# Kernel tuning notes

Measured on AMD Instinct MI355X. Metric: run time of the kernel, lower is better.

## Reference

```python
import jax, jax.numpy as jnp
import numpy as np

B, T, C, HS = 8, 4096, 1024, 64
HALF = HS // 2
ROPE_BASE = 10000.0


def _rope_tables(t_len, half_dim, base=ROPE_BASE):
    inv_freq = base ** (-jnp.arange(half_dim, dtype=jnp.float32) / half_dim)
    freqs = jnp.arange(t_len, dtype=jnp.float32)[:, None] * inv_freq[None, :]  # (T, D/2)
    return jnp.cos(freqs), jnp.sin(freqs)


def apply_rope(x, cos, sin):
    # x: (B, T, D) with interleaved even/odd pairs; cos/sin: (T, D/2)
    x_even = x[..., ::2]
    x_odd = x[..., 1::2]
    r_even = x_even * cos[None] - x_odd * sin[None]
    r_odd = x_even * sin[None] + x_odd * cos[None]
    # re-interleave
    return jnp.stack([r_even, r_odd], axis=-1).reshape(x.shape)


def setup_inputs() -> dict:
    key = jax.random.key(0)
    kx, kq, kk, kv = jax.random.split(key, 4)
    s = 1.0 / np.sqrt(C)
    cos, sin = _rope_tables(T, HALF)
    return {
        "x": jax.random.normal(kx, (B, T, C), dtype=jnp.float32),
        "cos": cos,
        "sin": sin,
        "Wq": jax.random.normal(kq, (C, HS), dtype=jnp.float32) * s,
        "Wk": jax.random.normal(kk, (C, HS), dtype=jnp.float32) * s,
        "Wv": jax.random.normal(kv, (C, HS), dtype=jnp.float32) * s,
    }


def reference(x, cos, sin, Wq, Wk, Wv):
    # q/k/v projections (bias-free Linear)
    q = jnp.einsum('btc,cd->btd', x, Wq)
    k = jnp.einsum('btc,cd->btd', x, Wk)
    v = jnp.einsum('btc,cd->btd', x, Wv)
    q = apply_rope(q, cos, sin)
    k = apply_rope(k, cos, sin)
    t = x.shape[1]
    scale = 1.0 / jnp.sqrt(jnp.asarray(k.shape[-1], dtype=x.dtype))
    wei = jnp.einsum('bqd,bkd->bqk', q, k) * scale  # (B, T, T)
    causal = jnp.tril(jnp.ones((t, t), dtype=bool))
    wei = jnp.where(causal[None], wei, -jnp.inf)
    wei = jax.nn.softmax(wei, axis=-1)
    # dropout = 0.0 (eval mode)
    return jnp.einsum('bqk,bkd->bqd', wei, v)
```

## Files before the change

kernel.cpp:

```cpp
#include <hip/hip_runtime.h>
#include <hip/hip_bf16.h>

#define BB 8
#define TT 4096
#define CC 1024
#define HS 64

typedef __attribute__((ext_vector_type(8))) __bf16 bf16x8;
typedef __attribute__((ext_vector_type(4))) __bf16 bf16x4;
typedef __attribute__((ext_vector_type(4))) float f32x4;

static __device__ __forceinline__ unsigned pack_bf16(float a, float b) {
    unsigned short ua = __builtin_bit_cast(unsigned short, (__bf16)a);
    unsigned short ub = __builtin_bit_cast(unsigned short, (__bf16)b);
    return (unsigned)ua | ((unsigned)ub << 16);
}

__global__ __launch_bounds__(256) void wprep_kernel(
    const float* __restrict__ Wq, const float* __restrict__ Wk,
    const float* __restrict__ Wv, __bf16* __restrict__ Wt)
{
    int i = blockIdx.x * 256 + threadIdx.x;
    int dr = i >> 10;
    int c  = i & 1023;
    int m  = dr >> 6;
    int d  = dr & 63;
    const float* src = (m == 0) ? Wq : ((m == 1) ? Wk : Wv);
    float v = src[(long)c * HS + d];
    if (m == 0) v *= 0.125f * 1.4426950408889634f;
    Wt[i] = (__bf16)v;
}

__global__ __launch_bounds__(256) void qkv_rope_kernel(
    const float* __restrict__ x,
    const float* __restrict__ cosT,
    const float* __restrict__ sinT,
    const __bf16* __restrict__ Wt,
    __bf16* __restrict__ Qo, __bf16* __restrict__ Ko, __bf16* __restrict__ Vo)
{
    __shared__ __bf16 xs[64][72];
    __shared__ __bf16 Wl[192][72];

    const int tid  = threadIdx.x;
    const int lane = tid & 63;
    const int w    = tid >> 6;
    const int col  = lane & 15;
    const int grp  = lane >> 4;
    const long rowbase = (long)blockIdx.x * 64;

    f32x4 acc[12];
#pragma unroll
    for (int i = 0; i < 12; i++) acc[i] = 0.0f;

    for (int ck = 0; ck < CC; ck += 64) {
        {
            int r = tid >> 2, c0 = (tid & 3) * 16;
            const float4* src = (const float4*)(x + (rowbase + r) * (long)CC + ck + c0);
#pragma unroll
            for (int i = 0; i < 4; i++) {
                float4 v = src[i];
                bf16x4 t;
                t[0] = (__bf16)v.x; t[1] = (__bf16)v.y;
                t[2] = (__bf16)v.z; t[3] = (__bf16)v.w;
                *(bf16x4*)&xs[r][c0 + i * 4] = t;
            }
        }
        {
#pragma unroll
            for (int i = 0; i < 6; i++) {
                int u = i * 256 + tid;
                int dr = u >> 3, cu = (u & 7) * 8;
                bf16x8 v = *(const bf16x8*)(Wt + (long)dr * CC + ck + cu);
                *(bf16x8*)&Wl[dr][cu] = v;
            }
        }
        __syncthreads();
#pragma unroll
        for (int s = 0; s < 2; s++) {
            bf16x8 a = *(const bf16x8*)&xs[w * 16 + col][s * 32 + grp * 8];
#pragma unroll
            for (int nf = 0; nf < 12; nf++) {
                bf16x8 b = *(const bf16x8*)&Wl[nf * 16 + col][s * 32 + grp * 8];
                acc[nf] = __builtin_amdgcn_mfma_f32_16x16x32_bf16(a, b, acc[nf], 0, 0, 0);
            }
        }
        __syncthreads();
    }

#pragma unroll
    for (int r = 0; r < 4; r++) {
        long grow = rowbase + w * 16 + grp * 4 + r;
        int t = (int)(grow & (TT - 1));
        const float* cp = cosT + (long)t * 32;
        const float* sp = sinT + (long)t * 32;
#pragma unroll
        for (int nf = 0; nf < 4; nf++) {
            int ii = nf * 8 + (col >> 1);
            float cs = cp[ii], sn = sp[ii];
            float sgn_sn = (col & 1) ? sn : -sn;
            float qv = acc[nf][r];
            float qp = __shfl_xor(qv, 1);
            float qo = qv * cs + qp * sgn_sn;
            float kv = acc[nf + 4][r];
            float kp = __shfl_xor(kv, 1);
            float ko = kv * cs + kp * sgn_sn;
            long base = grow * HS + nf * 16 + col;
            Qo[base] = (__bf16)qo;
            Ko[base] = (__bf16)ko;
            xs[nf * 16 + col][w * 16 + grp * 4 + r] = (__bf16)acc[nf + 8][r];
        }
    }
    __syncthreads();
    {
        int d = tid >> 2, seg = tid & 3;
        int b  = (int)(rowbase >> 12);
        int t0 = (int)(rowbase & (TT - 1));
        bf16x8 v0 = *(const bf16x8*)&xs[d][seg * 16];
        bf16x8 v1 = *(const bf16x8*)&xs[d][seg * 16 + 8];
        __bf16* dst = Vo + ((size_t)b * 64 + d) * TT + t0 + seg * 16;
        *(bf16x8*)dst = v0;
        *(bf16x8*)(dst + 8) = v1;
    }
}

__global__ __launch_bounds__(256, 2) void attn_kernel(
    const __bf16* __restrict__ Q, const __bf16* __restrict__ K,
    const __bf16* __restrict__ Vt, float* __restrict__ O)
{
    __shared__ __bf16 Kl[2][64 * 64];
    __shared__ __bf16 Vl[2][64 * 64];
    __shared__ __align__(16) unsigned char plds[4][2048];

    const int tid  = threadIdx.x;
    const int lane = tid & 63;
    const int col  = lane & 15;
    const int g    = lane >> 4;
    const int w    = tid >> 6;

    const int n  = blockIdx.x;
    const int b  = n & 7;
    const int k  = (n >> 3) & 31;
    const int qt = (n < 256) ? (63 - k) : k;

    const int qloc = qt * 64 + w * 16 + col;
    const size_t qrow = (size_t)b * TT + qloc;
    bf16x8 qb[2];
#pragma unroll
    for (int s = 0; s < 2; s++)
        qb[s] = *(const bf16x8*)(Q + qrow * HS + s * 32 + g * 8);

    const int r0 = tid >> 3, c0 = tid & 7;
    const int r1 = r0 + 32;
    const __bf16* Kbase = K + (size_t)b * TT * HS;
    const __bf16* Vbase = Vt + (size_t)b * 64 * TT;

#define SWZ(row, cb) (((row) << 6) | (((cb) ^ ((row) & 7)) << 3))

    f32x4 acc[4];
#pragma unroll
    for (int i = 0; i < 4; i++) acc[i] = 0.f;
    float mrun = -3e38f;
    float lsum0 = 0.f, lsum1 = 0.f, lsum2 = 0.f, lsum3 = 0.f;

    unsigned char* pbase = plds[w] + col * 128;
    const int sw = col & 7;

    bf16x8 sk0, sk1, sv0, sv1;
    auto stageLoad = [&](int j) {
        const __bf16* kp = Kbase + (size_t)(j * 64) * HS;
        sk0 = *(const bf16x8*)(kp + r0 * HS + c0 * 8);
        sk1 = *(const bf16x8*)(kp + r1 * HS + c0 * 8);
        const __bf16* vp = Vbase + j * 64;
        sv0 = *(const bf16x8*)(vp + (size_t)r0 * TT + c0 * 8);
        sv1 = *(const bf16x8*)(vp + (size_t)r1 * TT + c0 * 8);
    };
    auto stageWrite = [&](int buf) {
        *(bf16x8*)&Kl[buf][SWZ(r0, c0)] = sk0;
        *(bf16x8*)&Kl[buf][SWZ(r1, c0)] = sk1;
        *(bf16x8*)&Vl[buf][SWZ(r0, c0)] = sv0;
        *(bf16x8*)&Vl[buf][SWZ(r1, c0)] = sv1;
    };

    stageLoad(0);
    stageWrite(0);
    __syncthreads();

    int cur = 0;
    for (int j = 0; j <= qt; ++j) {
        const bool more = (j < qt);
        if (more) {
            stageLoad(j + 1);
        }
        __builtin_amdgcn_sched_barrier(0);

        f32x4 sf[4];
#pragma unroll
        for (int i = 0; i < 4; i++) sf[i] = 0.f;
        {
            bf16x8 kf[8];
#pragma unroll
            for (int nf = 0; nf < 4; nf++)
#pragma unroll
                for (int s = 0; s < 2; s++)
                    kf[nf * 2 + s] = *(const bf16x8*)&Kl[cur][SWZ(nf * 16 + col, s * 4 + g)];
            __builtin_amdgcn_s_setprio(1);
#pragma unroll
            for (int s = 0; s < 2; s++)
#pragma unroll
                for (int nf = 0; nf < 4; nf++)
                    sf[nf] = __builtin_amdgcn_mfma_f32_16x16x32_bf16(kf[nf * 2 + s], qb[s], sf[nf], 0, 0, 0);
            __builtin_amdgcn_s_setprio(0);
        }
        if (j == qt) {
#pragma unroll
            for (int nf = 0; nf < 4; nf++)
#pragma unroll
                for (int r = 0; r < 4; r++)
                    if (j * 64 + nf * 16 + g * 4 + r > qloc) sf[nf][r] = -3e38f;
        }
        float fm[4];
#pragma unroll
        for (int f = 0; f < 4; f++)
            fm[f] = fmaxf(fmaxf(sf[f][0], sf[f][1]), fmaxf(sf[f][2], sf[f][3]));
        float mt = fmaxf(fmaxf(fm[0], fm[1]), fmaxf(fm[2], fm[3]));
        if (!__all(mt <= mrun + 8.0f)) {
            float mg = fmaxf(mt, __shfl_xor(mt, 16));
            mg = fmaxf(mg, __shfl_xor(mg, 32));
            float mn = fmaxf(mrun, mg);
            float al = exp2f(mrun - mn);
            mrun = mn;
            lsum0 *= al; lsum1 *= al; lsum2 *= al; lsum3 *= al;
#pragma unroll
            for (int nf = 0; nf < 4; nf++) acc[nf] *= al;
        }
#pragma unroll
        for (int f = 0; f < 4; f++) {
            float p0 = exp2f(sf[f][0] - mrun);
            float p1 = exp2f(sf[f][1] - mrun);
            float p2 = exp2f(sf[f][2] - mrun);
            float p3 = exp2f(sf[f][3] - mrun);
            sf[f][0] = p0; sf[f][1] = p1; sf[f][2] = p2; sf[f][3] = p3;
            lsum0 += p0; lsum1 += p1; lsum2 += p2; lsum3 += p3;
        }
#pragma unroll
        for (int nf = 0; nf < 4; nf++) {
            uint2 val;
            val.x = pack_bf16(sf[nf][0], sf[nf][1]);
            val.y = pack_bf16(sf[nf][2], sf[nf][3]);
            *(uint2*)(pbase + ((((nf * 2 + (g >> 1)) ^ sw) << 4) | ((g & 1) << 3))) = val;
        }
        {
            bf16x8 vf[8];
#pragma unroll
            for (int nf = 0; nf < 4; nf++)
#pragma unroll
                for (int s = 0; s < 2; s++)
                    vf[nf * 2 + s] = *(const bf16x8*)&Vl[cur][SWZ(nf * 16 + col, s * 4 + g)];
            __builtin_amdgcn_s_setprio(1);
#pragma unroll
            for (int s = 0; s < 2; s++) {
                bf16x8 pf = *(const bf16x8*)(pbase + (((s * 4 + g) ^ sw) << 4));
#pragma unroll
                for (int nf = 0; nf < 4; nf++)
                    acc[nf] = __builtin_amdgcn_mfma_f32_16x16x32_bf16(vf[nf * 2 + s], pf, acc[nf], 0, 0, 0);
            }
            __builtin_amdgcn_s_setprio(0);
        }
        if (more) {
            stageWrite(cur ^ 1);
        }
        __syncthreads();
        cur ^= 1;
    }

    float ls = (lsum0 + lsum1) + (lsum2 + lsum3);
    ls += __shfl_xor(ls, 16);
    ls += __shfl_xor(ls, 32);
    float rinv = __builtin_amdgcn_rcpf(ls);
    float* orow = O + qrow * HS;
#pragma unroll
    for (int nf = 0; nf < 4; nf++) {
        float4 v;
        v.x = acc[nf][0] * rinv; v.y = acc[nf][1] * rinv;
        v.z = acc[nf][2] * rinv; v.w = acc[nf][3] * rinv;
        *(float4*)(orow + nf * 16 + g * 4) = v;
    }
#undef SWZ
}

extern "C" void kernel_launch(void* const* d_in, const int* in_sizes, int n_in,
                              void* d_out, int out_size, void* d_ws, size_t ws_size,
                              hipStream_t stream)
{
    const float* x    = (const float*)d_in[0];
    const float* cosT = (const float*)d_in[1];
    const float* sinT = (const float*)d_in[2];
    const float* Wq   = (const float*)d_in[3];
    const float* Wk   = (const float*)d_in[4];
    const float* Wv   = (const float*)d_in[5];
    float* out = (float*)d_out;

    __bf16* Qb = (__bf16*)d_ws;
    __bf16* Kb = Qb + (size_t)BB * TT * HS;
    __bf16* Vb = Kb + (size_t)BB * TT * HS;
    __bf16* Wt = Vb + (size_t)BB * TT * HS;

    wprep_kernel<<<(192 * 1024) / 256, 256, 0, stream>>>(Wq, Wk, Wv, Wt);
    qkv_rope_kernel<<<(BB * TT) / 64, 256, 0, stream>>>(x, cosT, sinT, Wt, Qb, Kb, Vb);
    attn_kernel<<<512, 256, 0, stream>>>(Qb, Kb, Vb, out);
}
```

Measured before the change: 90.99 us.

## Split long causal query tiles across two blocks and merge with a combine kernel

Query tiles 32-63 have their key range split into two chunks (keys 0-31 and 32..qt), each run by its own block. Each of those blocks writes an unnormalised partial output plus its running max and sum, and a new combine kernel merges the two with log-sum-exp weights. This raises the grid from 512 to 768 more evenly sized blocks, and launch bounds go to 3 blocks per SM to improve load balance and occupancy. The cost is extra global traffic for the partials, one extra kernel launch, and possible register spills from the tighter launch bound.

```diff
diff --git a/kernel.cpp b/kernel.cpp
--- a/kernel.cpp
+++ b/kernel.cpp
@@ -123,9 +123,10 @@
     }
 }
 
-__global__ __launch_bounds__(256, 2) void attn_kernel(
+__global__ __launch_bounds__(256, 3) void attn_kernel(
     const __bf16* __restrict__ Q, const __bf16* __restrict__ K,
-    const __bf16* __restrict__ Vt, float* __restrict__ O)
+    const __bf16* __restrict__ Vt, float* __restrict__ O,
+    float* __restrict__ Opart, float* __restrict__ mlbuf)
 {
     __shared__ __bf16 Kl[2][64 * 64];
     __shared__ __bf16 Vl[2][64 * 64];
@@ -137,10 +138,14 @@
     const int g    = lane >> 4;
     const int w    = tid >> 6;
 
-    const int n  = blockIdx.x;
-    const int b  = n & 7;
-    const int k  = (n >> 3) & 31;
-    const int qt = (n < 256) ? (63 - k) : k;
+    const int n   = blockIdx.x;
+    const int b   = n & 7;
+    const int idx = n >> 3;
+    int qt, j0, j1, ch;
+    bool partial;
+    if (idx < 32)      { qt = 32 + idx;  j0 = 0;  j1 = 32;     partial = true;  ch = 0; }
+    else if (idx < 64) { qt = idx;       j0 = 32; j1 = qt + 1; partial = true;  ch = 1; }
+    else               { qt = 95 - idx;  j0 = 0;  j1 = qt + 1; partial = false; ch = 0; }
 
     const int qloc = qt * 64 + w * 16 + col;
     const size_t qrow = (size_t)b * TT + qloc;
@@ -181,13 +186,13 @@
         *(bf16x8*)&Vl[buf][SWZ(r1, c0)] = sv1;
     };
 
-    stageLoad(0);
+    stageLoad(j0);
     stageWrite(0);
     __syncthreads();
 
     int cur = 0;
-    for (int j = 0; j <= qt; ++j) {
-        const bool more = (j < qt);
+    for (int j = j0; j < j1; ++j) {
+        const bool more = (j + 1 < j1);
         if (more) {
             stageLoad(j + 1);
         }
@@ -276,16 +281,67 @@
     float ls = (lsum0 + lsum1) + (lsum2 + lsum3);
     ls += __shfl_xor(ls, 16);
     ls += __shfl_xor(ls, 32);
-    float rinv = __builtin_amdgcn_rcpf(ls);
-    float* orow = O + qrow * HS;
-#pragma unroll
-    for (int nf = 0; nf < 4; nf++) {
+
+    if (!partial) {
+        float rinv = __builtin_amdgcn_rcpf(ls);
+        float* orow = O + qrow * HS;
+#pragma unroll
+        for (int nf = 0; nf < 4; nf++) {
+            float4 v;
+            v.x = acc[nf][0] * rinv; v.y = acc[nf][1] * rinv;
+            v.z = acc[nf][2] * rinv; v.w = acc[nf][3] * rinv;
+            *(float4*)(orow + nf * 16 + g * 4) = v;
+        }
+    } else {
+        const int slot = (b * 32 + (qt - 32)) * 2 + ch;
+        float* prow = Opart + ((size_t)slot * 64 + w * 16 + col) * 64;
+#pragma unroll
+        for (int nf = 0; nf < 4; nf++) {
+            float4 v;
+            v.x = acc[nf][0]; v.y = acc[nf][1];
+            v.z = acc[nf][2]; v.w = acc[nf][3];
+            *(float4*)(prow + nf * 16 + g * 4) = v;
+        }
+        if (g == 0) {
+            float2 mv = make_float2(mrun, ls);
+            *(float2*)(mlbuf + ((size_t)slot * 64 + w * 16 + col) * 2) = mv;
+        }
+    }
+#undef SWZ
+}
+
+__global__ __launch_bounds__(256) void combine_kernel(
+    const float* __restrict__ Opart, const float* __restrict__ mlbuf,
+    float* __restrict__ O)
+{
+    const int qi = blockIdx.x;
+    const int b  = blockIdx.y;
+    const int row = threadIdx.x >> 2;
+    const int seg = threadIdx.x & 3;
+    const int slot0 = (b * 32 + qi) * 2;
+
+    const float* p0 = mlbuf + ((size_t)slot0 * 64 + row) * 2;
+    const float* p1 = mlbuf + ((size_t)(slot0 + 1) * 64 + row) * 2;
+    float m0 = p0[0], l0 = p0[1];
+    float m1 = p1[0], l1 = p1[1];
+    float M  = fmaxf(m0, m1);
+    float w0 = exp2f(m0 - M), w1 = exp2f(m1 - M);
+    float rinv = 1.0f / (l0 * w0 + l1 * w1);
+    w0 *= rinv; w1 *= rinv;
+
+    const float4* s0 = (const float4*)(Opart + ((size_t)slot0 * 64 + row) * 64 + seg * 16);
+    const float4* s1 = (const float4*)(Opart + ((size_t)(slot0 + 1) * 64 + row) * 64 + seg * 16);
+    float4* dst = (float4*)(O + ((size_t)b * TT + (32 + qi) * 64 + row) * 64 + seg * 16);
+#pragma unroll
+    for (int i = 0; i < 4; i++) {
+        float4 a = s0[i], c = s1[i];
         float4 v;
-        v.x = acc[nf][0] * rinv; v.y = acc[nf][1] * rinv;
-        v.z = acc[nf][2] * rinv; v.w = acc[nf][3] * rinv;
-        *(float4*)(orow + nf * 16 + g * 4) = v;
-    }
-#undef SWZ
+        v.x = a.x * w0 + c.x * w1;
+        v.y = a.y * w0 + c.y * w1;
+        v.z = a.z * w0 + c.z * w1;
+        v.w = a.w * w0 + c.w * w1;
+        dst[i] = v;
+    }
 }
 
 extern "C" void kernel_launch(void* const* d_in, const int* in_sizes, int n_in,
@@ -305,7 +361,12 @@
     __bf16* Vb = Kb + (size_t)BB * TT * HS;
     __bf16* Wt = Vb + (size_t)BB * TT * HS;
 
+    const size_t base_bytes = (size_t)3 * BB * TT * HS * 2 + 192 * 1024 * 2;
+    float* Opart = (float*)((char*)d_ws + ((base_bytes + 255) & ~(size_t)255));
+    float* mlbuf = Opart + (size_t)8 * 32 * 2 * 64 * 64;
+
     wprep_kernel<<<(192 * 1024) / 256, 256, 0, stream>>>(Wq, Wk, Wv, Wt);
     qkv_rope_kernel<<<(BB * TT) / 64, 256, 0, stream>>>(x, cosT, sinT, Wt, Qb, Kb, Vb);
-    attn_kernel<<<512, 256, 0, stream>>>(Qb, Kb, Vb, out);
-}
+    attn_kernel<<<768, 256, 0, stream>>>(Qb, Kb, Vb, out, Opart, mlbuf);
+    combine_kernel<<<dim3(32, 8), 256, 0, stream>>>(Opart, mlbuf, out);
+}
```

Result: no change. 89.69 us (-1.4%).

## Split attention KV range into two chunks per 128-row Q tile with combine kernel

Applied to the files above, without the earlier changes.

Each attention block now handles 128 query rows (two 16-row sub-tiles per wave) so every K/V tile staged into LDS is reused by twice as many queries. The KV range of each Q tile is split into two halves processed by separate blocks, which balances causal work across the 512 blocks. The blocks write fp16 partial outputs plus max/sum statistics, and a new combine kernel merges them. This adds a kernel launch, extra global traffic for the partials, and fp16 rounding of the intermediate outputs.

```diff
diff --git a/kernel.cpp b/kernel.cpp
--- a/kernel.cpp
+++ b/kernel.cpp
@@ -14,6 +14,14 @@
     unsigned short ua = __builtin_bit_cast(unsigned short, (__bf16)a);
     unsigned short ub = __builtin_bit_cast(unsigned short, (__bf16)b);
     return (unsigned)ua | ((unsigned)ub << 16);
+}
+static __device__ __forceinline__ unsigned pack_f16(float a, float b) {
+    unsigned short ua = __builtin_bit_cast(unsigned short, (_Float16)a);
+    unsigned short ub = __builtin_bit_cast(unsigned short, (_Float16)b);
+    return (unsigned)ua | ((unsigned)ub << 16);
+}
+static __device__ __forceinline__ float h2f(unsigned short u) {
+    return (float)__builtin_bit_cast(_Float16, u);
 }
 
 __global__ __launch_bounds__(256) void wprep_kernel(
@@ -125,11 +133,12 @@
 
 __global__ __launch_bounds__(256, 2) void attn_kernel(
     const __bf16* __restrict__ Q, const __bf16* __restrict__ K,
-    const __bf16* __restrict__ Vt, float* __restrict__ O)
+    const __bf16* __restrict__ Vt,
+    _Float16* __restrict__ Opart, float* __restrict__ mlbuf)
 {
     __shared__ __bf16 Kl[2][64 * 64];
     __shared__ __bf16 Vl[2][64 * 64];
-    __shared__ __align__(16) unsigned char plds[4][2048];
+    __shared__ __align__(16) unsigned char plds[4][2][2048];
 
     const int tid  = threadIdx.x;
     const int lane = tid & 63;
@@ -137,17 +146,21 @@
     const int g    = lane >> 4;
     const int w    = tid >> 6;
 
-    const int n  = blockIdx.x;
-    const int b  = n & 7;
-    const int k  = (n >> 3) & 31;
-    const int qt = (n < 256) ? (63 - k) : k;
-
-    const int qloc = qt * 64 + w * 16 + col;
-    const size_t qrow = (size_t)b * TT + qloc;
-    bf16x8 qb[2];
-#pragma unroll
-    for (int s = 0; s < 2; s++)
-        qb[s] = *(const bf16x8*)(Q + qrow * HS + s * 32 + g * 8);
+    const int n = blockIdx.x;
+    const int b = n & 7;
+    const int j_ = n >> 3;
+    int Qt, ch, j0, j1;
+    if (j_ < 32) { Qt = 31 - j_; ch = 0; j0 = 0;      j1 = Qt + 1; }
+    else         { Qt = j_ - 32; ch = 1; j0 = Qt + 1; j1 = 2 * Qt + 2; }
+
+    const int qbase = Qt * 128 + w * 32;
+    const size_t qgrow = (size_t)b * TT + qbase;
+    bf16x8 qb[2][2];
+#pragma unroll
+    for (int sub = 0; sub < 2; sub++)
+#pragma unroll
+        for (int s = 0; s < 2; s++)
+            qb[sub][s] = *(const bf16x8*)(Q + (qgrow + sub * 16 + col) * HS + s * 32 + g * 8);
 
     const int r0 = tid >> 3, c0 = tid & 7;
     const int r1 = r0 + 32;
@@ -156,13 +169,14 @@
 
 #define SWZ(row, cb) (((row) << 6) | (((cb) ^ ((row) & 7)) << 3))
 
-    f32x4 acc[4];
-#pragma unroll
-    for (int i = 0; i < 4; i++) acc[i] = 0.f;
-    float mrun = -3e38f;
-    float lsum0 = 0.f, lsum1 = 0.f, lsum2 = 0.f, lsum3 = 0.f;
-
-    unsigned char* pbase = plds[w] + col * 128;
+    f32x4 acc[2][4];
+#pragma unroll
+    for (int sub = 0; sub < 2; sub++)
+#pragma unroll
+        for (int i = 0; i < 4; i++) acc[sub][i] = 0.f;
+    float mrun[2] = { -3e38f, -3e38f };
+    float lsum[2][4] = { {0.f,0.f,0.f,0.f}, {0.f,0.f,0.f,0.f} };
+
     const int sw = col & 7;
 
     bf16x8 sk0, sk1, sv0, sv1;
@@ -181,111 +195,170 @@
         *(bf16x8*)&Vl[buf][SWZ(r1, c0)] = sv1;
     };
 
-    stageLoad(0);
+    stageLoad(j0);
     stageWrite(0);
     __syncthreads();
 
     int cur = 0;
-    for (int j = 0; j <= qt; ++j) {
-        const bool more = (j < qt);
-        if (more) {
-            stageLoad(j + 1);
-        }
+    for (int j = j0; j < j1; ++j) {
+        const bool more = (j + 1 < j1);
+        if (more) stageLoad(j + 1);
         __builtin_amdgcn_sched_barrier(0);
 
-        f32x4 sf[4];
-#pragma unroll
-        for (int i = 0; i < 4; i++) sf[i] = 0.f;
-        {
-            bf16x8 kf[8];
-#pragma unroll
-            for (int nf = 0; nf < 4; nf++)
-#pragma unroll
-                for (int s = 0; s < 2; s++)
-                    kf[nf * 2 + s] = *(const bf16x8*)&Kl[cur][SWZ(nf * 16 + col, s * 4 + g)];
+        bf16x8 kf[8];
+#pragma unroll
+        for (int nf = 0; nf < 4; nf++)
+#pragma unroll
+            for (int s = 0; s < 2; s++)
+                kf[nf * 2 + s] = *(const bf16x8*)&Kl[cur][SWZ(nf * 16 + col, s * 4 + g)];
+
+#pragma unroll
+        for (int sub = 0; sub < 2; sub++) {
+            if (j * 64 > qbase + sub * 16) continue;
+            f32x4 sf[4];
+#pragma unroll
+            for (int i = 0; i < 4; i++) sf[i] = 0.f;
             __builtin_amdgcn_s_setprio(1);
 #pragma unroll
             for (int s = 0; s < 2; s++)
 #pragma unroll
                 for (int nf = 0; nf < 4; nf++)
-                    sf[nf] = __builtin_amdgcn_mfma_f32_16x16x32_bf16(kf[nf * 2 + s], qb[s], sf[nf], 0, 0, 0);
+                    sf[nf] = __builtin_amdgcn_mfma_f32_16x16x32_bf16(kf[nf * 2 + s], qb[sub][s], sf[nf], 0, 0, 0);
             __builtin_amdgcn_s_setprio(0);
-        }
-        if (j == qt) {
-#pragma unroll
-            for (int nf = 0; nf < 4; nf++)
-#pragma unroll
-                for (int r = 0; r < 4; r++)
-                    if (j * 64 + nf * 16 + g * 4 + r > qloc) sf[nf][r] = -3e38f;
-        }
-        float fm[4];
-#pragma unroll
-        for (int f = 0; f < 4; f++)
-            fm[f] = fmaxf(fmaxf(sf[f][0], sf[f][1]), fmaxf(sf[f][2], sf[f][3]));
-        float mt = fmaxf(fmaxf(fm[0], fm[1]), fmaxf(fm[2], fm[3]));
-        if (!__all(mt <= mrun + 8.0f)) {
-            float mg = fmaxf(mt, __shfl_xor(mt, 16));
-            mg = fmaxf(mg, __shfl_xor(mg, 32));
-            float mn = fmaxf(mrun, mg);
-            float al = exp2f(mrun - mn);
-            mrun = mn;
-            lsum0 *= al; lsum1 *= al; lsum2 *= al; lsum3 *= al;
-#pragma unroll
-            for (int nf = 0; nf < 4; nf++) acc[nf] *= al;
-        }
-#pragma unroll
-        for (int f = 0; f < 4; f++) {
-            float p0 = exp2f(sf[f][0] - mrun);
-            float p1 = exp2f(sf[f][1] - mrun);
-            float p2 = exp2f(sf[f][2] - mrun);
-            float p3 = exp2f(sf[f][3] - mrun);
-            sf[f][0] = p0; sf[f][1] = p1; sf[f][2] = p2; sf[f][3] = p3;
-            lsum0 += p0; lsum1 += p1; lsum2 += p2; lsum3 += p3;
-        }
-#pragma unroll
-        for (int nf = 0; nf < 4; nf++) {
-            uint2 val;
-            val.x = pack_bf16(sf[nf][0], sf[nf][1]);
-            val.y = pack_bf16(sf[nf][2], sf[nf][3]);
-            *(uint2*)(pbase + ((((nf * 2 + (g >> 1)) ^ sw) << 4) | ((g & 1) << 3))) = val;
-        }
-        {
-            bf16x8 vf[8];
-#pragma unroll
-            for (int nf = 0; nf < 4; nf++)
-#pragma unroll
-                for (int s = 0; s < 2; s++)
-                    vf[nf * 2 + s] = *(const bf16x8*)&Vl[cur][SWZ(nf * 16 + col, s * 4 + g)];
+            if (j >= 2 * Qt) {
+                const int qloc = qbase + sub * 16 + col;
+#pragma unroll
+                for (int nf = 0; nf < 4; nf++)
+#pragma unroll
+                    for (int r = 0; r < 4; r++)
+                        if (j * 64 + nf * 16 + g * 4 + r > qloc) sf[nf][r] = -3e38f;
+            }
+            float fm[4];
+#pragma unroll
+            for (int f = 0; f < 4; f++)
+                fm[f] = fmaxf(fmaxf(sf[f][0], sf[f][1]), fmaxf(sf[f][2], sf[f][3]));
+            float mt = fmaxf(fmaxf(fm[0], fm[1]), fmaxf(fm[2], fm[3]));
+            if (!__all(mt <= mrun[sub] + 8.0f)) {
+                float mg = fmaxf(mt, __shfl_xor(mt, 16));
+                mg = fmaxf(mg, __shfl_xor(mg, 32));
+                float mn = fmaxf(mrun[sub], mg);
+                float al = exp2f(mrun[sub] - mn);
+                mrun[sub] = mn;
+#pragma unroll
+                for (int q = 0; q < 4; q++) lsum[sub][q] *= al;
+#pragma unroll
+                for (int nf = 0; nf < 4; nf++) acc[sub][nf] *= al;
+            }
+#pragma unroll
+            for (int f = 0; f < 4; f++) {
+                float p0 = exp2f(sf[f][0] - mrun[sub]);
+                float p1 = exp2f(sf[f][1] - mrun[sub]);
+                float p2 = exp2f(sf[f][2] - mrun[sub]);
+                float p3 = exp2f(sf[f][3] - mrun[sub]);
+                sf[f][0] = p0; sf[f][1] = p1; sf[f][2] = p2; sf[f][3] = p3;
+                lsum[sub][0] += p0; lsum[sub][1] += p1;
+                lsum[sub][2] += p2; lsum[sub][3] += p3;
+            }
+            unsigned char* pb = &plds[w][sub][0] + col * 128;
+#pragma unroll
+            for (int nf = 0; nf < 4; nf++) {
+                uint2 val;
+                val.x = pack_bf16(sf[nf][0], sf[nf][1]);
+                val.y = pack_bf16(sf[nf][2], sf[nf][3]);
+                *(uint2*)(pb + ((((nf * 2 + (g >> 1)) ^ sw) << 4) | ((g & 1) << 3))) = val;
+            }
+        }
+
+        bf16x8 vf[8];
+#pragma unroll
+        for (int nf = 0; nf < 4; nf++)
+#pragma unroll
+            for (int s = 0; s < 2; s++)
+                vf[nf * 2 + s] = *(const bf16x8*)&Vl[cur][SWZ(nf * 16 + col, s * 4 + g)];
+
+#pragma unroll
+        for (int sub = 0; sub < 2; sub++) {
+            if (j * 64 > qbase + sub * 16) continue;
+            unsigned char* pb = &plds[w][sub][0] + col * 128;
             __builtin_amdgcn_s_setprio(1);
 #pragma unroll
             for (int s = 0; s < 2; s++) {
-                bf16x8 pf = *(const bf16x8*)(pbase + (((s * 4 + g) ^ sw) << 4));
+                bf16x8 pf = *(const bf16x8*)(pb + (((s * 4 + g) ^ sw) << 4));
 #pragma unroll
                 for (int nf = 0; nf < 4; nf++)
-                    acc[nf] = __builtin_amdgcn_mfma_f32_16x16x32_bf16(vf[nf * 2 + s], pf, acc[nf], 0, 0, 0);
+                    acc[sub][nf] = __builtin_amdgcn_mfma_f32_16x16x32_bf16(vf[nf * 2 + s], pf, acc[sub][nf], 0, 0, 0);
             }
             __builtin_amdgcn_s_setprio(0);
         }
-        if (more) {
-            stageWrite(cur ^ 1);
-        }
+
+        if (more) stageWrite(cur ^ 1);
         __syncthreads();
         cur ^= 1;
     }
 
-    float ls = (lsum0 + lsum1) + (lsum2 + lsum3);
-    ls += __shfl_xor(ls, 16);
-    ls += __shfl_xor(ls, 32);
-    float rinv = __builtin_amdgcn_rcpf(ls);
-    float* orow = O + qrow * HS;
-#pragma unroll
-    for (int nf = 0; nf < 4; nf++) {
+    const size_t slot = (size_t)(b * 32 + Qt) * 2 + ch;
+#pragma unroll
+    for (int sub = 0; sub < 2; sub++) {
+        float ls = (lsum[sub][0] + lsum[sub][1]) + (lsum[sub][2] + lsum[sub][3]);
+        ls += __shfl_xor(ls, 16);
+        ls += __shfl_xor(ls, 32);
+        float rinv = (ls > 0.f) ? __builtin_amdgcn_rcpf(ls) : 0.f;
+        const int rowg = w * 32 + sub * 16 + col;
+        _Float16* prow = Opart + slot * 8192 + (size_t)rowg * 64;
+#pragma unroll
+        for (int nf = 0; nf < 4; nf++) {
+            uint2 v;
+            v.x = pack_f16(acc[sub][nf][0] * rinv, acc[sub][nf][1] * rinv);
+            v.y = pack_f16(acc[sub][nf][2] * rinv, acc[sub][nf][3] * rinv);
+            *(uint2*)(prow + nf * 16 + g * 4) = v;
+        }
+        if (g == 0) {
+            float2 mv = make_float2(mrun[sub], ls);
+            *(float2*)(mlbuf + (slot * 128 + rowg) * 2) = mv;
+        }
+    }
+#undef SWZ
+}
+
+__global__ __launch_bounds__(256) void combine_kernel(
+    const _Float16* __restrict__ Opart, const float* __restrict__ mlbuf,
+    float* __restrict__ O)
+{
+    const int Qt = blockIdx.x;
+    const int b  = blockIdx.y;
+    const int row = threadIdx.x >> 1;
+    const int seg = threadIdx.x & 1;
+    const size_t slot0 = (size_t)(b * 32 + Qt) * 2;
+
+    const float* p0 = mlbuf + ((slot0 + 0) * 128 + row) * 2;
+    const float* p1 = mlbuf + ((slot0 + 1) * 128 + row) * 2;
+    float m0 = p0[0], l0 = p0[1];
+    float m1 = p1[0], l1 = p1[1];
+    float M  = fmaxf(m0, m1);
+    float w0 = l0 * exp2f(m0 - M);
+    float w1 = l1 * exp2f(m1 - M);
+    float rinv = 1.0f / (w0 + w1);
+    w0 *= rinv; w1 *= rinv;
+
+    const uint4* s0 = (const uint4*)(Opart + (slot0 + 0) * 8192 + (size_t)row * 64 + seg * 32);
+    const uint4* s1 = (const uint4*)(Opart + (slot0 + 1) * 8192 + (size_t)row * 64 + seg * 32);
+    float* dst = O + ((size_t)b * TT + Qt * 128 + row) * 64 + seg * 32;
+#pragma unroll
+    for (int i = 0; i < 4; i++) {
+        uint4 a = s0[i], c = s1[i];
         float4 v;
-        v.x = acc[nf][0] * rinv; v.y = acc[nf][1] * rinv;
-        v.z = acc[nf][2] * rinv; v.w = acc[nf][3] * rinv;
-        *(float4*)(orow + nf * 16 + g * 4) = v;
-    }
-#undef SWZ
+        v.x = h2f((unsigned short)(a.x      )) * w0 + h2f((unsigned short)(c.x      )) * w1;
+        v.y = h2f((unsigned short)(a.x >> 16)) * w0 + h2f((unsigned short)(c.x >> 16)) * w1;
+        v.z = h2f((unsigned short)(a.y      )) * w0 + h2f((unsigned short)(c.y      )) * w1;
+        v.w = h2f((unsigned short)(a.y >> 16)) * w0 + h2f((unsigned short)(c.y >> 16)) * w1;
+        *(float4*)(dst + i * 8) = v;
+        float4 u;
+        u.x = h2f((unsigned short)(a.z      )) * w0 + h2f((unsigned short)(c.z      )) * w1;
+        u.y = h2f((unsigned short)(a.z >> 16)) * w0 + h2f((unsigned short)(c.z >> 16)) * w1;
+        u.z = h2f((unsigned short)(a.w      )) * w0 + h2f((unsigned short)(c.w      )) * w1;
+        u.w = h2f((unsigned short)(a.w >> 16)) * w0 + h2f((unsigned short)(c.w >> 16)) * w1;
+        *(float4*)(dst + i * 8 + 4) = u;
+    }
 }
 
 extern "C" void kernel_launch(void* const* d_in, const int* in_sizes, int n_in,
@@ -305,7 +378,12 @@
     __bf16* Vb = Kb + (size_t)BB * TT * HS;
     __bf16* Wt = Vb + (size_t)BB * TT * HS;
 
+    const size_t base_bytes = (size_t)3 * BB * TT * HS * 2 + 192 * 1024 * 2;
+    _Float16* Opart = (_Float16*)((char*)d_ws + ((base_bytes + 255) & ~(size_t)255));
+    float* mlbuf = (float*)(Opart + (size_t)512 * 8192);
+
     wprep_kernel<<<(192 * 1024) / 256, 256, 0, stream>>>(Wq, Wk, Wv, Wt);
     qkv_rope_kernel<<<(BB * TT) / 64, 256, 0, stream>>>(x, cosT, sinT, Wt, Qb, Kb, Vb);
-    attn_kernel<<<512, 256, 0, stream>>>(Qb, Kb, Vb, out);
-}
+    attn_kernel<<<512, 256, 0, stream>>>(Qb, Kb, Vb, Opart, mlbuf);
+    combine_kernel<<<dim3(32, 8), 256, 0, stream>>>(Opart, mlbuf, out);
+}
```

Measured after the change: 101.7 us. 11.8% more time.
